# Performance work log

Measured on AMD Instinct MI355X. Metric: run time of the kernel, lower is better.

The kernel has to match this reference:

```python
import jax, jax.numpy as jnp
import numpy as np

PAD, BOS = 0, 1
EPS = 1e-08


def _lstm_cell(xt, h, c, wih, whh, bih, bhh):
    z = xt @ wih.T + h @ whh.T + bih + bhh
    i, f, g, o = jnp.split(z, 4, axis=-1)  # torch gate order i,f,g,o
    c = jax.nn.sigmoid(f) * c + jax.nn.sigmoid(i) * jnp.tanh(g)
    h = jax.nn.sigmoid(o) * jnp.tanh(c)
    return h, c


def _run_lstm(emb, wih, whh, bih, bhh):
    B, H = emb.shape[0], whh.shape[1]
    def step(carry, xt):
        h, c = _lstm_cell(xt, carry[0], carry[1], wih, whh, bih, bhh)
        return (h, c), h
    init = (jnp.zeros((B, H), emb.dtype), jnp.zeros((B, H), emb.dtype))
    (hT, cT), outs = jax.lax.scan(step, init, jnp.swapaxes(emb, 0, 1))
    return jnp.swapaxes(outs, 0, 1), hT, cT


def setup_inputs() -> dict:
    key = jax.random.key(0)
    V, H, B, S, T = 32000, 256, 8, 200, 51
    ks = jax.random.split(key, 24)
    def n(i, shape, s=0.02):
        return jax.random.normal(ks[i], shape, jnp.float32) * s
    x = jax.random.randint(ks[0], (B, S), 1, V)
    x = x.at[:, -1].set(V - 1)  # pins extended vocab size to 2V
    labels = jax.random.randint(ks[1], (B, T), 1, V)
    return {
        "x": x, "labels": labels, "ext_vocab_size": 2 * V,
        "emb_enc": n(2, (V, H)).at[PAD].set(0.0),
        "wih_f": n(3, (4 * H, H)), "whh_f": n(4, (4 * H, H)),
        "bih_f": jnp.zeros((4 * H,), jnp.float32), "bhh_f": jnp.zeros((4 * H,), jnp.float32),
        "wih_b": n(5, (4 * H, H)), "whh_b": n(6, (4 * H, H)),
        "bih_b": jnp.zeros((4 * H,), jnp.float32), "bhh_b": jnp.zeros((4 * H,), jnp.float32),
        "w_sel1": n(7, (H, 2 * H)), "b_sel1": jnp.zeros((H,), jnp.float32),
        "w_sel2": n(8, (1, H)), "b_sel2": jnp.zeros((1,), jnp.float32),
        "w_rh": n(9, (H, 2 * H)), "b_rh": jnp.zeros((H,), jnp.float32),
        "w_rc": n(10, (H, 2 * H)), "b_rc": jnp.zeros((H,), jnp.float32),
        "emb_dec": n(11, (V, H)).at[PAD].set(0.0),
        "wih_d": n(12, (4 * H, 3 * H)), "whh_d": n(13, (4 * H, H)),
        "bih_d": jnp.zeros((4 * H,), jnp.float32), "bhh_d": jnp.zeros((4 * H,), jnp.float32),
        "w_attn": n(14, (H, 4 * H)), "b_attn": jnp.zeros((H,), jnp.float32),
        "w_attn_v": n(15, (1, H)),
        "w_ptr": n(16, (1, 3 * H)), "b_ptr": jnp.zeros((1,), jnp.float32),
        "w_gen": n(17, (V, H)), "b_gen": jnp.zeros((V,), jnp.float32),
        "w_cov": n(18, (H, 1)), "b_cov": jnp.zeros((H,), jnp.float32),
    }


def reference(x, labels, ext_vocab_size, emb_enc, wih_f, whh_f, bih_f, bhh_f,
              wih_b, whh_b, bih_b, bhh_b, w_sel1, b_sel1, w_sel2, b_sel2,
              w_rh, b_rh, w_rc, b_rc, emb_dec, wih_d, whh_d, bih_d, bhh_d,
              w_attn, b_attn, w_attn_v, w_ptr, b_ptr, w_gen, b_gen, w_cov, b_cov):
    B, S = x.shape
    V, H = w_gen.shape
    # ---- Encoder: BiLSTM (no padding -> packing is identity; eval -> no dropout)
    emb = emb_enc[x]  # [B,S,H]
    out_f, h_f, c_f = _run_lstm(emb, wih_f, whh_f, bih_f, bhh_f)
    out_b_r, h_b, c_b = _run_lstm(emb[:, ::-1], wih_b, whh_b, bih_b, bhh_b)
    enc_out = jnp.concatenate([out_f, out_b_r[:, ::-1]], axis=-1)  # [B,S,2H]
    copy_probs = jax.nn.sigmoid(
        (jnp.tanh(enc_out @ w_sel1.T + b_sel1) @ w_sel2.T + b_sel2)[..., 0])  # [B,S]
    # ---- bidirectional state reduction
    h0 = jax.nn.relu(jnp.concatenate([h_f, h_b], -1) @ w_rh.T + b_rh)
    c0 = jax.nn.relu(jnp.concatenate([c_f, c_b], -1) @ w_rc.T + b_rc)
    # ---- Decoder loop (teacher forcing): inputs = [BOS, labels[:,1:T-1]]
    dec_in = jnp.concatenate(
        [jnp.full((B, 1), BOS, labels.dtype), labels[:, 1:-1]], axis=1)  # [B,T-1]
    mask_cp = (copy_probs > EPS).astype(jnp.float32)
    rows = jnp.arange(B)[:, None]

    def step(carry, tok):
        h, c, cov = carry
        cov_feat = cov[..., None] * w_cov[:, 0] + b_cov  # [B,S,H]
        feats = jnp.concatenate(
            [enc_out, jnp.broadcast_to(h[:, None, :], (B, S, H)), cov_feat], axis=-1)
        e = jnp.tanh(feats @ w_attn.T + b_attn)           # [B,S,H]
        attn = jax.nn.softmax(e @ w_attn_v[0], axis=1)    # [B,S]
        attn = attn * mask_cp
        attn = attn / (attn.sum(1, keepdims=True) + 1e-10)
        cov = cov + attn
        ctx = jnp.einsum('bs,bsd->bd', attn, enc_out)     # [B,2H]
        h, c = _lstm_cell(jnp.concatenate([emb_dec[tok], ctx], -1), h, c,
                          wih_d, whh_d, bih_d, bhh_d)
        p_gen = jax.nn.sigmoid(jnp.concatenate([ctx, h], -1) @ w_ptr.T + b_ptr)  # [B,1]
        vocab_dist = jax.nn.softmax(h @ w_gen.T + b_gen, axis=-1)  # [B,V]
        dist = jnp.zeros((B, ext_vocab_size), jnp.float32)
        dist = dist.at[:, :V].set(p_gen * vocab_dist)
        dist = dist.at[rows, x].add((1.0 - p_gen) * attn)  # pointer/copy scatter-add
        return (h, c, cov), dist

    cov0 = jnp.zeros((B, S), jnp.float32)
    _, outs = jax.lax.scan(step, (h0, c0, cov0), dec_in.T)
    outputs = jnp.swapaxes(outs, 0, 1)  # [B,T-1,EV]
    # ---- loss (faithful: CE treats the mixture distribution as logits)
    targets = labels[:, 1:]
    logp = jax.nn.log_softmax(outputs, axis=-1)
    nll = -jnp.take_along_axis(logp, targets[..., None], axis=-1)[..., 0]
    valid = (targets != PAD).astype(jnp.float32)
    loss_ce = (nll * valid).sum() / valid.sum()
    m = (x != PAD).astype(jnp.float32)
    lp = jnp.clip(jnp.log(copy_probs), -100.0, None)
    l1p = jnp.clip(jnp.log1p(-copy_probs), -100.0, None)
    bce = -(m * lp + (1.0 - m) * l1p)
    loss = loss_ce + 1.0 * (bce * m).sum() / m.sum()
    return outputs, loss
```

## Files before the change

### kernel.cpp

```cpp
#include <hip/hip_runtime.h>
#include <hip/hip_bf16.h>
#include <stdint.h>


#define DEVI __device__ __forceinline__
#define AT_RLX __ATOMIC_RELAXED
#define SC_AGT __HIP_MEMORY_SCOPE_AGENT

static constexpr size_t OFF_ACC   = 0;
static constexpr size_t OFF_FLAGE = 4;
static constexpr size_t OFF_FLAGD = 36;
static constexpr size_t ZERO_FLOATS = 200;
static constexpr size_t OFF_CTX   = 256;
static constexpr size_t OFF_EMB   = 4352;
static constexpr size_t OFF_HSEL  = OFF_EMB;
static constexpr size_t OFF_HP    = OFF_EMB;
static constexpr size_t OFF_PREF  = OFF_EMB  + 409600;
static constexpr size_t OFF_PREB  = OFF_PREF + 1638400;
static constexpr size_t OFF_BIAS  = OFF_PREB + 1638400;
static constexpr size_t OFF_HB    = OFF_BIAS + 3072;
static constexpr size_t OFF_HFIN  = OFF_HB   + 8192;
static constexpr size_t OFF_CFIN  = OFF_HFIN + 4096;
static constexpr size_t OFF_ENCOUT= OFF_CFIN + 4096;
static constexpr size_t OFF_MASK  = OFF_ENCOUT + 819200;
static constexpr size_t OFF_C0    = OFF_MASK + 1600;
static constexpr size_t OFF_EP    = OFF_C0   + 2048;
static constexpr size_t OFF_WCP   = OFF_EP   + 409600;
static constexpr size_t OFF_BCP   = OFF_WCP  + 256;
static constexpr size_t OFF_DEMB  = OFF_BCP  + 256;
static constexpr size_t OFF_DPRE  = OFF_DEMB + 102400;
static constexpr size_t OFF_HBUF  = OFF_DPRE + 409600;
static constexpr size_t OFF_CS    = OFF_HBUF + 4096;
static constexpr size_t OFF_HS    = OFF_CS   + 204800;
static constexpr size_t OFF_AS    = OFF_HS   + 102400;
static constexpr size_t OFF_PG    = OFF_AS   + 80000;
static constexpr size_t OFF_PE    = OFF_PG   + 512;

DEVI float sigf(float x)      { return 1.0f / (1.0f + __expf(-x)); }
DEVI float tanh_fast(float x) { return 1.0f - 2.0f / (1.0f + __expf(2.0f * x)); }
DEVI float ald(const float* p)  { return __hip_atomic_load((float*)p, AT_RLX, SC_AGT); }
DEVI void  ast(float* p, float v){ __hip_atomic_store(p, v, AT_RLX, SC_AGT); }

DEVI void fbar(int* flags, int g, int n, int val) {
  __syncthreads();
  if ((int)threadIdx.x == 0)
    __hip_atomic_store(flags + g, val, AT_RLX, SC_AGT);
  if ((int)threadIdx.x < n && (int)threadIdx.x != g) {
    while (__hip_atomic_load(flags + threadIdx.x, AT_RLX, SC_AGT) < val)
      __builtin_amdgcn_s_sleep(1);
  }
  __syncthreads();
}

__global__ __launch_bounds__(256) void k_biassum(
    const float* bih_f, const float* bhh_f, const float* bih_b, const float* bhh_b,
    const float* bih_d, const float* bhh_d, float* ws) {
  int i = blockIdx.x * 256 + threadIdx.x;
  int which = i >> 10, jj = i & 1023;
  float v = (which == 0) ? bih_f[jj] + bhh_f[jj]
          : (which == 1) ? bih_b[jj] + bhh_b[jj]
                         : bih_d[jj] + bhh_d[jj];
  ws[OFF_BIAS + i] = v;
}

__global__ __launch_bounds__(256) void k_embed(
    const int* xin, const int* labels, const float* emb_enc, const float* emb_dec, float* ws) {
  int r = blockIdx.x, h = threadIdx.x;
  if (r < 1600) {
    int t = r >> 3, b = r & 7;
    ws[OFF_EMB + (size_t)r * 256 + h] = emb_enc[(size_t)xin[b * 200 + t] * 256 + h];
  } else {
    int r2 = r - 1600;
    int t = r2 >> 3, b = r2 & 7;
    int tok = (t == 0) ? 1 : labels[b * 51 + t];
    ws[OFF_DEMB + (size_t)r2 * 256 + h] = emb_dec[(size_t)tok * 256 + h];
  }
}

template<int BM, int BN, int TM, int TN, int CMAP, int ACT, int AMAP>
__global__ __launch_bounds__(256) void k_gemm(
    const float* __restrict__ A, const float* __restrict__ B,
    const float* __restrict__ bias, float* __restrict__ C,
    int M, int K, int ldb, int ldc) {
  __shared__ float As[16][BM];
  __shared__ float Bs[16][BN];
  const int tid = threadIdx.x;
  const int tx = tid & 15, ty = tid >> 4;
  const int m0 = blockIdx.x * BM, n0 = blockIdx.y * BN;
  float acc[TM][TN];
#pragma unroll
  for (int i = 0; i < TM; ++i)
#pragma unroll
    for (int q = 0; q < TN; ++q) acc[i][q] = 0.f;

  for (int kk = 0; kk < K; kk += 16) {
#pragma unroll
    for (int e = tid; e < BM * 4; e += 256) {
      int m = e >> 2, k4 = (e & 3) * 4;
      int gm0 = m0 + m;
      float4 v = {0.f, 0.f, 0.f, 0.f};
      if (gm0 < M) {
        int gm = AMAP ? (((199 - (gm0 >> 3)) << 3) + (gm0 & 7)) : gm0;
        v = *(const float4*)(A + (size_t)gm * K + kk + k4);
      }
      As[k4 + 0][m] = v.x; As[k4 + 1][m] = v.y; As[k4 + 2][m] = v.z; As[k4 + 3][m] = v.w;
    }
#pragma unroll
    for (int e = tid; e < BN * 4; e += 256) {
      int n = e >> 2, k4 = (e & 3) * 4;
      float4 v = *(const float4*)(B + (size_t)(n0 + n) * ldb + kk + k4);
      Bs[k4 + 0][n] = v.x; Bs[k4 + 1][n] = v.y; Bs[k4 + 2][n] = v.z; Bs[k4 + 3][n] = v.w;
    }
    __syncthreads();
#pragma unroll
    for (int k = 0; k < 16; ++k) {
      float a[TM], bv[TN];
#pragma unroll
      for (int i = 0; i < TM; ++i) a[i] = As[k][ty * TM + i];
#pragma unroll
      for (int q = 0; q < TN; ++q) bv[q] = Bs[k][tx * TN + q];
#pragma unroll
      for (int i = 0; i < TM; ++i)
#pragma unroll
        for (int q = 0; q < TN; ++q) acc[i][q] += a[i] * bv[q];
    }
    __syncthreads();
  }
#pragma unroll
  for (int i = 0; i < TM; ++i) {
    int gm = m0 + ty * TM + i;
    if (gm >= M) continue;
    size_t base;
    if (CMAP == 1) { int t = gm >> 3, b = gm & 7; base = (size_t)(b * 50 + t) * 64000; }
    else            base = (size_t)gm * ldc;
#pragma unroll
    for (int q = 0; q < TN; ++q) {
      int n = n0 + tx * TN + q;
      float v = acc[i][q] + bias[n];
      if (ACT == 1) v = tanh_fast(v);
      C[base + n] = v;
    }
  }
}

__global__ __launch_bounds__(512, 1) void k_encoder(
    const float* __restrict__ whh_f, const float* __restrict__ whh_b, float* __restrict__ ws) {
  __shared__ float hs[8 * 288];
  __shared__ float zs[512];
  const int dir = blockIdx.x >> 4;
  const int p   = blockIdx.x & 15;
  const int u0  = p * 16;
  const float* whh = dir ? whh_b : whh_f;
  const float* pre = ws + (dir ? OFF_PREB : OFF_PREF);
  unsigned long long* hp = (unsigned long long*)(ws + OFF_HP);
  const int tid = threadIdx.x;
  const int r = tid >> 3, kc = tid & 7;
  const int gt = r >> 4, ui = r & 15;
  const int j = gt * 256 + u0 + ui;
  float4 W[8];
  {
    const float* wr = whh + (size_t)j * 256 + kc * 32;
#pragma unroll
    for (int q = 0; q < 8; ++q) W[q] = *(const float4*)(wr + q * 4);
  }
  const int ui2 = tid & 15, b2 = tid >> 4;
  float c_reg = 0.f;
  float* enc = ws + OFF_ENCOUT;

  for (int t = 0; t < 200; ++t) {
    float pre_v = pre[((size_t)t * 8 + kc) * 1024 + j];
    float acc[8];
#pragma unroll
    for (int b = 0; b < 8; ++b) acc[b] = 0.f;
    if (t > 0) {
      {
        unsigned long long* src = hp + (size_t)((((t + 1) & 1) * 2 + dir) * 2048) + tid * 4;
        const unsigned long long e = (unsigned long long)(unsigned)t;
        unsigned long long a0, a1, a2, a3;
        for (;;) {
          a0 = __hip_atomic_load(src + 0, AT_RLX, SC_AGT);
          a1 = __hip_atomic_load(src + 1, AT_RLX, SC_AGT);
          a2 = __hip_atomic_load(src + 2, AT_RLX, SC_AGT);
          a3 = __hip_atomic_load(src + 3, AT_RLX, SC_AGT);
          if (((a0 >> 32) == e) && ((a1 >> 32) == e) &&
              ((a2 >> 32) == e) && ((a3 >> 32) == e)) break;
          __builtin_amdgcn_s_sleep(1);
        }
        int kk0 = (tid * 4) & 255, bb = tid >> 6;
        float* dst = &hs[bb * 288 + (kk0 >> 5) * 36 + (kk0 & 31)];
        dst[0] = __uint_as_float((unsigned)a0);
        dst[1] = __uint_as_float((unsigned)a1);
        dst[2] = __uint_as_float((unsigned)a2);
        dst[3] = __uint_as_float((unsigned)a3);
      }
      __syncthreads();
      const float* hrow = &hs[kc * 36];
#pragma unroll
      for (int b = 0; b < 8; ++b) {
        const float* hbp = hrow + b * 288;
#pragma unroll
        for (int q = 0; q < 8; ++q) {
          float4 h4 = *(const float4*)(hbp + q * 4);
          acc[b] = fmaf(W[q].x, h4.x, acc[b]);
          acc[b] = fmaf(W[q].y, h4.y, acc[b]);
          acc[b] = fmaf(W[q].z, h4.z, acc[b]);
          acc[b] = fmaf(W[q].w, h4.w, acc[b]);
        }
      }
    }
    {
      bool h4b = (kc & 4) != 0;
#pragma unroll
      for (int i = 0; i < 4; ++i) {
        float send = h4b ? acc[i] : acc[i + 4];
        float keep = h4b ? acc[i + 4] : acc[i];
        acc[i] = keep + __shfl_xor(send, 4);
      }
      bool h2b = (kc & 2) != 0;
#pragma unroll
      for (int i = 0; i < 2; ++i) {
        float send = h2b ? acc[i] : acc[i + 2];
        float keep = h2b ? acc[i + 2] : acc[i];
        acc[i] = keep + __shfl_xor(send, 2);
      }
      bool h1b = (kc & 1) != 0;
      {
        float send = h1b ? acc[0] : acc[1];
        float keep = h1b ? acc[1] : acc[0];
        acc[0] = keep + __shfl_xor(send, 1);
      }
    }
    zs[tid] = acc[0] + pre_v;
    __syncthreads();
    if (tid < 128) {
      int i0 = ui2 * 8 + b2;
      float zi = zs[i0], zf = zs[128 + i0], zg = zs[256 + i0], zo = zs[384 + i0];
      float cn = sigf(zf) * c_reg + sigf(zi) * tanh_fast(zg);
      float hn = sigf(zo) * tanh_fast(cn);
      c_reg = cn;
      int uu = u0 + ui2;
      if (t < 199) {
        unsigned long long pk =
            ((unsigned long long)(unsigned)(t + 1) << 32) |
            (unsigned long long)__float_as_uint(hn);
        __hip_atomic_store(hp + (size_t)(((t & 1) * 2 + dir) * 2048) + b2 * 256 + uu,
                           pk, AT_RLX, SC_AGT);
      }
      int s = dir ? (199 - t) : t;
      enc[((size_t)b2 * 200 + s) * 512 + dir * 256 + uu] = hn;
      if (t == 199) {
        ws[OFF_HFIN + (size_t)(dir * 8 + b2) * 256 + uu] = hn;
        ws[OFF_CFIN + (size_t)(dir * 8 + b2) * 256 + uu] = cn;
      }
    }
  }
}

__global__ __launch_bounds__(64) void k_selbce(
    const float* w_sel2, const float* b_sel2, const int* xin, float* ws) {
  int r = blockIdx.x, lane = threadIdx.x;
  float pacc = 0.f;
#pragma unroll
  for (int i = 0; i < 4; ++i) {
    int k = lane + 64 * i;
    pacc += ws[OFF_HSEL + (size_t)r * 256 + k] * w_sel2[k];
  }
#pragma unroll
  for (int m = 1; m < 64; m <<= 1) pacc += __shfl_xor(pacc, m);
  if (lane == 0) {
    float cp = sigf(pacc + b_sel2[0]);
    ws[OFF_MASK + r] = (cp > 1e-8f) ? 1.f : 0.f;
    int b = r / 200, s = r % 200;
    float m = (xin[b * 200 + s] != 0) ? 1.f : 0.f;
    if (m > 0.f) {
      float lp = fmaxf(logf(cp), -100.f);
      atomicAdd(ws + OFF_ACC + 2, -lp);
    }
    atomicAdd(ws + OFF_ACC + 3, m);
  }
}

__global__ __launch_bounds__(256) void k_wcp(
    const float* w_attn, const float* w_cov, const float* b_cov, float* ws) {
  int jj = threadIdx.x;
  float a = 0.f, c = 0.f;
  for (int h = 0; h < 256; ++h) {
    float w = w_attn[(size_t)jj * 1024 + 768 + h];
    a += w * w_cov[h];
    c += w * b_cov[h];
  }
  ws[OFF_WCP + jj] = a;
  ws[OFF_BCP + jj] = c;
}

__global__ __launch_bounds__(256) void k_h0c0(
    const float* w_rh, const float* b_rh, const float* w_rc, const float* b_rc, float* ws) {
  int b = blockIdx.x, jj = threadIdx.x;
  const float* hf  = ws + OFF_HFIN + (size_t)b * 256;
  const float* hbk = ws + OFF_HFIN + 2048 + (size_t)b * 256;
  const float* cf  = ws + OFF_CFIN + (size_t)b * 256;
  const float* cbk = ws + OFF_CFIN + 2048 + (size_t)b * 256;
  float ah = b_rh[jj], ac = b_rc[jj];
  for (int k = 0; k < 256; ++k) {
    ah += hf[k] * w_rh[(size_t)jj * 512 + k];
    ac += cf[k] * w_rc[(size_t)jj * 512 + k];
  }
  for (int k = 0; k < 256; ++k) {
    ah += hbk[k] * w_rh[(size_t)jj * 512 + 256 + k];
    ac += cbk[k] * w_rc[(size_t)jj * 512 + 256 + k];
  }
  ws[OFF_C0 + (size_t)b * 256 + jj] = fmaxf(ac, 0.f);
  ws[OFF_HBUF + (size_t)b * 256 + jj] = fmaxf(ah, 0.f);
}

__global__ __launch_bounds__(512, 1) void k_decoder(
    const float* __restrict__ wih_d, const float* __restrict__ whh_d,
    const float* __restrict__ w_attn, const float* __restrict__ w_attn_v,
    float* __restrict__ ws) {
  __shared__ float hc_s[8 * 768];
  __shared__ float h_pad[264];
  __shared__ float hw_q[64];
  __shared__ float e_s[256];
  __shared__ float at_s[256], cv_s[256], msk_s[256];
  __shared__ float zs_l[256];
  __shared__ float wcq_s[64], bcq_s[64], wvq_s[64];
  __shared__ float mS_s[2];
  const int g = blockIdx.x, tid = threadIdx.x;
  const int b1 = g >> 2, sq = g & 3, s0 = sq * 50;
  int* flags = (int*)(ws + OFF_FLAGD);
  const int jl = tid >> 3, kq = tid & 7;
  const int kseg = tid & 15, row_l = tid >> 4;
  const int u_l = row_l & 7, gate = row_l >> 3;
  const int j = gate * 256 + g * 8 + u_l;
  float4 W48[12];
#pragma unroll
  for (int q = 0; q < 12; ++q) {
    int k0 = 4 * kseg + 64 * q;
    W48[q] = (k0 < 512) ? *(const float4*)(wih_d + (size_t)j * 768 + 256 + k0)
                        : *(const float4*)(whh_d + (size_t)j * 256 + (k0 - 512));
  }
  float4 W32[8];
  {
    const float* wsrc = w_attn + (size_t)(sq * 64 + jl) * 1024 + 512 + kq * 32;
#pragma unroll
    for (int q = 0; q < 8; ++q) W32[q] = *(const float4*)(wsrc + q * 4);
  }
  const int u_c = tid & 7, b_c = tid >> 3;
  float c_reg = (tid < 64) ? ws[OFF_C0 + (size_t)b_c * 256 + g * 8 + u_c] : 0.f;
  for (int s = tid; s < 256; s += 512) {
    msk_s[s] = (s < 200) ? ws[OFF_MASK + b1 * 200 + s] : 0.f;
    cv_s[s] = 0.f;
  }
  if (tid < 64) {
    wcq_s[tid] = ws[OFF_WCP + sq * 64 + tid];
    bcq_s[tid] = ws[OFF_BCP + sq * 64 + tid];
    wvq_s[tid] = w_attn_v[sq * 64 + tid];
  }
  __syncthreads();

  for (int t = 0; t < 50; ++t) {
    const int rb = t & 1, wb = 1 - rb;
    if (tid < 128) ast(ws + OFF_CTX + g * 128 + tid, 0.f);
    if (tid < 256) {
      float v = ald(ws + OFF_HBUF + (size_t)rb * 2048 + b1 * 256 + tid);
      h_pad[(tid >> 5) * 33 + (tid & 31)] = v;
    }
    __syncthreads();
    {
      float a = 0.f;
      const float* hq = &h_pad[kq * 33];
#pragma unroll
      for (int q = 0; q < 8; ++q) {
        float4 h4 = { hq[q * 4 + 0], hq[q * 4 + 1], hq[q * 4 + 2], hq[q * 4 + 3] };
        a = fmaf(W32[q].x, h4.x, a);
        a = fmaf(W32[q].y, h4.y, a);
        a = fmaf(W32[q].z, h4.z, a);
        a = fmaf(W32[q].w, h4.w, a);
      }
      a += __shfl_xor(a, 1);
      a += __shfl_xor(a, 2);
      a += __shfl_xor(a, 4);
      if (kq == 0) hw_q[jl] = a;
    }
    __syncthreads();
    if (tid < 200) {
      const int s = tid;
      float cv = cv_s[s];
      const float* ep = ws + OFF_EP + ((size_t)(b1 * 200 + s)) * 256 + sq * 64;
      float pe = 0.f;
#pragma unroll
      for (int i4 = 0; i4 < 16; ++i4) {
        float4 e4 = *(const float4*)(ep + i4 * 4);
        float4 h4 = *(const float4*)(&hw_q[i4 * 4]);
        float4 w4 = *(const float4*)(&wcq_s[i4 * 4]);
        float4 b4 = *(const float4*)(&bcq_s[i4 * 4]);
        float4 v4 = *(const float4*)(&wvq_s[i4 * 4]);
        pe = fmaf(tanh_fast(e4.x + h4.x + cv * w4.x + b4.x), v4.x, pe);
        pe = fmaf(tanh_fast(e4.y + h4.y + cv * w4.y + b4.y), v4.y, pe);
        pe = fmaf(tanh_fast(e4.z + h4.z + cv * w4.z + b4.z), v4.z, pe);
        pe = fmaf(tanh_fast(e4.w + h4.w + cv * w4.w + b4.w), v4.w, pe);
      }
      ast(ws + OFF_PE + (size_t)(sq * 8 + b1) * 200 + s, pe);
    }
    fbar(flags, g, 32, 3 * t + 1);

    if (tid < 200) {
      float e0 = ald(ws + OFF_PE + (size_t)(0 * 8 + b1) * 200 + tid);
      float e1 = ald(ws + OFF_PE + (size_t)(1 * 8 + b1) * 200 + tid);
      float e2 = ald(ws + OFF_PE + (size_t)(2 * 8 + b1) * 200 + tid);
      float e3 = ald(ws + OFF_PE + (size_t)(3 * 8 + b1) * 200 + tid);
      e_s[tid] = (e0 + e1) + (e2 + e3);
    }
    __syncthreads();
    if (tid < 64) {
      float m = -1e30f;
#pragma unroll
      for (int i = 0; i < 4; ++i) {
        int s = tid + 64 * i;
        if (s < 200) m = fmaxf(m, e_s[s]);
      }
#pragma unroll
      for (int md = 1; md < 64; md <<= 1) m = fmaxf(m, __shfl_xor(m, md));
      float es = 0.f, ems = 0.f;
#pragma unroll
      for (int i = 0; i < 4; ++i) {
        int s = tid + 64 * i;
        if (s < 200) {
          float e = __expf(e_s[s] - m);
          es += e; ems += e * msk_s[s];
        }
      }
#pragma unroll
      for (int md = 1; md < 64; md <<= 1) { es += __shfl_xor(es, md); ems += __shfl_xor(ems, md); }
      if (tid == 0) { mS_s[0] = m; mS_s[1] = 1.0f / (ems + 1e-10f * es); }
    }
    __syncthreads();
    if (tid < 200) {
      float a = __expf(e_s[tid] - mS_s[0]) * msk_s[tid] * mS_s[1];
      at_s[tid] = a;
      cv_s[tid] += a;
      if (tid >= s0 && tid < s0 + 50)
        ws[OFF_AS + ((size_t)t * 8 + b1) * 200 + tid] = a;
    }
    __syncthreads();
    {
      float ca = 0.f;
      const float* ebase = ws + OFF_ENCOUT + ((size_t)(b1 * 200 + s0)) * 512 + tid;
#pragma unroll 10
      for (int s2 = 0; s2 < 50; ++s2)
        ca = fmaf(at_s[s0 + s2], ebase[(size_t)s2 * 512], ca);
      atomicAdd(ws + OFF_CTX + b1 * 512 + tid, ca);
    }
    fbar(flags, g, 32, 3 * t + 2);

    for (int e = tid; e < 6144; e += 512) {
      int bb = e / 768, kk2 = e % 768;
      hc_s[e] = (kk2 < 512) ? ald(ws + OFF_CTX + bb * 512 + kk2)
                            : ald(ws + OFF_HBUF + (size_t)rb * 2048 + bb * 256 + (kk2 - 512));
    }
    __syncthreads();
    if (g < 8) ws[OFF_CS + ((size_t)t * 8 + g) * 512 + tid] = hc_s[g * 768 + tid];
    float acc[8];
#pragma unroll
    for (int b = 0; b < 8; ++b) acc[b] = 0.f;
#pragma unroll
    for (int q = 0; q < 12; ++q) {
      int k0 = 4 * kseg + 64 * q;
#pragma unroll
      for (int b = 0; b < 8; ++b) {
        float4 h4 = *(const float4*)(&hc_s[b * 768 + k0]);
        acc[b] = fmaf(W48[q].x, h4.x, acc[b]);
        acc[b] = fmaf(W48[q].y, h4.y, acc[b]);
        acc[b] = fmaf(W48[q].z, h4.z, acc[b]);
        acc[b] = fmaf(W48[q].w, h4.w, acc[b]);
      }
    }
    {
      bool h8 = (kseg & 8) != 0;
#pragma unroll
      for (int i = 0; i < 4; ++i) {
        float send = h8 ? acc[i] : acc[i + 4];
        float keep = h8 ? acc[i + 4] : acc[i];
        acc[i] = keep + __shfl_xor(send, 8);
      }
      bool h4b = (kseg & 4) != 0;
#pragma unroll
      for (int i = 0; i < 2; ++i) {
        float send = h4b ? acc[i] : acc[i + 2];
        float keep = h4b ? acc[i + 2] : acc[i];
        acc[i] = keep + __shfl_xor(send, 4);
      }
      bool h2b = (kseg & 2) != 0;
      {
        float send = h2b ? acc[0] : acc[1];
        float keep = h2b ? acc[1] : acc[0];
        acc[0] = keep + __shfl_xor(send, 2);
      }
      acc[0] += __shfl_xor(acc[0], 1);
    }
    {
      int bz = kseg >> 1;
      float z = acc[0] + ws[OFF_DPRE + ((size_t)t * 8 + bz) * 1024 + j];
      if ((kseg & 1) == 0) zs_l[row_l * 8 + bz] = z;
    }
    __syncthreads();
    if (tid < 64) {
      float zi = zs_l[(0  + u_c) * 8 + b_c];
      float zf = zs_l[(8  + u_c) * 8 + b_c];
      float zg = zs_l[(16 + u_c) * 8 + b_c];
      float zo = zs_l[(24 + u_c) * 8 + b_c];
      float cn = sigf(zf) * c_reg + sigf(zi) * tanh_fast(zg);
      float hn = sigf(zo) * tanh_fast(cn);
      c_reg = cn;
      ast(ws + OFF_HBUF + (size_t)wb * 2048 + b_c * 256 + g * 8 + u_c, hn);
      ws[OFF_HS + ((size_t)t * 8 + b_c) * 256 + g * 8 + u_c] = hn;
    }
    fbar(flags, g, 32, 3 * t + 3);
  }
}

__global__ __launch_bounds__(64) void k_pgen(const float* w_ptr, const float* b_ptr, float* ws) {
  int r = blockIdx.x, lane = threadIdx.x;
  float p = 0.f;
#pragma unroll
  for (int i = 0; i < 12; ++i) {
    int k = lane + 64 * i;
    float v = (k < 512) ? ws[OFF_CS + (size_t)r * 512 + k]
                        : ws[OFF_HS + (size_t)r * 256 + (k - 512)];
    p += v * w_ptr[k];
  }
#pragma unroll
  for (int m = 1; m < 64; m <<= 1) p += __shfl_xor(p, m);
  if (lane == 0) ws[OFF_PG + r] = sigf(p + b_ptr[0]);
}

__global__ __launch_bounds__(256) void k_v2(const int* xin, const int* labels, float* ws, float* out) {
  __shared__ float redm[256], reds[256];
  __shared__ int xv[200];
  __shared__ float s1sh, corrsh;
  int r = blockIdx.x, tid = threadIdx.x;
  int tt = r >> 3, b = r & 7;
  float* row = out + (size_t)(b * 50 + tt) * 64000;
  for (int i = tid; i < 200; i += 256) xv[i] = xin[b * 200 + i];
  float m = -1e30f, s = 0.f;
  for (int i = tid; i < 32000; i += 256) {
    float z = row[i];
    float nm = fmaxf(m, z);
    s = s * __expf(m - nm) + __expf(z - nm);
    m = nm;
  }
  redm[tid] = m; reds[tid] = s;
  __syncthreads();
  for (int st = 128; st >= 1; st >>= 1) {
    if (tid < st) {
      float m2 = redm[tid + st], s2 = reds[tid + st];
      float M = fmaxf(redm[tid], m2);
      reds[tid] = reds[tid] * __expf(redm[tid] - M) + s2 * __expf(m2 - M);
      redm[tid] = M;
    }
    __syncthreads();
  }
  float mx = redm[0], sum = reds[0];
  float pg = ws[OFF_PG + r];
  __syncthreads();
  float s1 = 0.f;
  float inv = 1.0f / sum;
  for (int i = tid; i < 32000; i += 256) {
    float z = row[i];
    float d = pg * (__expf(z - mx) * inv);
    row[i] = d;
    s1 += __expf(d);
  }
  for (int i = 32000 + tid; i < 64000; i += 256) row[i] = 0.0f;
  reds[tid] = s1;
  __syncthreads();
  for (int st = 128; st >= 1; st >>= 1) { if (tid < st) reds[tid] += reds[tid + st]; __syncthreads(); }
  if (tid == 0) { s1sh = reds[0]; corrsh = 0.f; }
  __syncthreads();
  if (tid < 200) {
    int v = xv[tid];
    bool own = true;
    for (int s2 = 0; s2 < tid; ++s2) if (xv[s2] == v) { own = false; break; }
    if (own) {
      float delta = 0.f;
      for (int s2 = tid; s2 < 200; ++s2)
        if (xv[s2] == v) delta += ws[OFF_AS + (size_t)r * 200 + s2];
      delta *= (1.0f - pg);
      float base = row[v];
      row[v] = base + delta;
      atomicAdd(&corrsh, __expf(base + delta) - __expf(base));
    }
  }
  __syncthreads();
  if (tid == 0) {
    float lse = logf(s1sh + corrsh + 32000.0f);
    int tgt = labels[b * 51 + tt + 1];
    float dt = row[tgt];
    float valid = (tgt != 0) ? 1.f : 0.f;
    atomicAdd(ws + OFF_ACC + 0, valid * (lse - dt));
    atomicAdd(ws + OFF_ACC + 1, valid);
  }
}

__global__ void k_loss(float* ws, float* out, int out_size) {
  out[out_size - 1] = ws[OFF_ACC + 0] / ws[OFF_ACC + 1] + ws[OFF_ACC + 2] / ws[OFF_ACC + 3];
}

extern "C" void kernel_launch(void* const* d_in, const int* in_sizes, int n_in,
                              void* d_out, int out_size, void* d_ws, size_t ws_size,
                              hipStream_t stream) {
  (void)in_sizes; (void)n_in; (void)ws_size;
  const int*   x       = (const int*)  d_in[0];
  const int*   labels  = (const int*)  d_in[1];
  const float* emb_enc = (const float*)d_in[3];
  const float* wih_f   = (const float*)d_in[4];
  const float* whh_f   = (const float*)d_in[5];
  const float* bih_f   = (const float*)d_in[6];
  const float* bhh_f   = (const float*)d_in[7];
  const float* wih_b   = (const float*)d_in[8];
  const float* whh_b   = (const float*)d_in[9];
  const float* bih_b   = (const float*)d_in[10];
  const float* bhh_b   = (const float*)d_in[11];
  const float* w_sel1  = (const float*)d_in[12];
  const float* b_sel1  = (const float*)d_in[13];
  const float* w_sel2  = (const float*)d_in[14];
  const float* b_sel2  = (const float*)d_in[15];
  const float* w_rh    = (const float*)d_in[16];
  const float* b_rh    = (const float*)d_in[17];
  const float* w_rc    = (const float*)d_in[18];
  const float* b_rc    = (const float*)d_in[19];
  const float* emb_dec = (const float*)d_in[20];
  const float* wih_d   = (const float*)d_in[21];
  const float* whh_d   = (const float*)d_in[22];
  const float* bih_d   = (const float*)d_in[23];
  const float* bhh_d   = (const float*)d_in[24];
  const float* w_attn  = (const float*)d_in[25];
  const float* b_attn  = (const float*)d_in[26];
  const float* w_attn_v= (const float*)d_in[27];
  const float* w_ptr   = (const float*)d_in[28];
  const float* b_ptr   = (const float*)d_in[29];
  const float* w_gen   = (const float*)d_in[30];
  const float* b_gen   = (const float*)d_in[31];
  const float* w_cov   = (const float*)d_in[32];
  const float* b_cov   = (const float*)d_in[33];
  float* ws  = (float*)d_ws;
  float* out = (float*)d_out;

  hipMemsetAsync(d_ws, 0, ZERO_FLOATS * 4, stream);
  k_biassum<<<12, 256, 0, stream>>>(bih_f, bhh_f, bih_b, bhh_b, bih_d, bhh_d, ws);
  k_embed<<<2000, 256, 0, stream>>>(x, labels, emb_enc, emb_dec, ws);
  k_gemm<64,64,4,4,0,0,0><<<dim3(25,16), 256, 0, stream>>>(ws+OFF_EMB,  wih_f, ws+OFF_BIAS,      ws+OFF_PREF, 1600, 256, 256, 1024);
  k_gemm<64,64,4,4,0,0,1><<<dim3(25,16), 256, 0, stream>>>(ws+OFF_EMB,  wih_b, ws+OFF_BIAS+1024, ws+OFF_PREB, 1600, 256, 256, 1024);
  k_gemm<64,64,4,4,0,0,0><<<dim3(7,16),  256, 0, stream>>>(ws+OFF_DEMB, wih_d, ws+OFF_BIAS+2048, ws+OFF_DPRE, 400,  256, 768, 1024);
  hipMemsetAsync((void*)(ws + OFF_HP), 0, (size_t)2 * 2 * 2048 * sizeof(unsigned long long), stream);
  k_encoder<<<32, 512, 0, stream>>>(whh_f, whh_b, ws);
  k_gemm<64,64,4,4,0,1,0><<<dim3(25,4),  256, 0, stream>>>(ws+OFF_ENCOUT, w_sel1, b_sel1, ws+OFF_HSEL, 1600, 512, 512, 256);
  k_selbce<<<1600, 64, 0, stream>>>(w_sel2, b_sel2, x, ws);
  k_gemm<64,64,4,4,0,0,0><<<dim3(25,4),  256, 0, stream>>>(ws+OFF_ENCOUT, w_attn, b_attn, ws+OFF_EP, 1600, 512, 1024, 256);
  k_wcp<<<1, 256, 0, stream>>>(w_attn, w_cov, b_cov, ws);
  k_h0c0<<<8, 256, 0, stream>>>(w_rh, b_rh, w_rc, b_rc, ws);
  k_decoder<<<32, 512, 0, stream>>>(wih_d, whh_d, w_attn, w_attn_v, ws);
  k_pgen<<<400, 64, 0, stream>>>(w_ptr, b_ptr, ws);
  k_gemm<128,128,8,8,1,0,0><<<dim3(4,250), 256, 0, stream>>>(ws+OFF_HS, w_gen, b_gen, out, 400, 256, 256, 64000);
  k_v2<<<400, 256, 0, stream>>>(x, labels, ws, out);
  k_loss<<<1, 1, 0, stream>>>(ws, out, out_size);
}
```

Measured before the change: 2.314 ms.

## Remap encoder recurrence threads to two gate rows and sixteen k-chunks

Restructures the encoder LSTM recurrent matvec so each thread holds two weight rows over a 16-wide k-slice instead of one row over 32, and reuses each shared-memory h vector load for both rows. The shared h buffer gets an interleaved layout, and the butterfly reduction grows an extra shuffle stage over 16 lanes. The aim is to halve LDS reads per FMA on the serial 200-step critical path, at the cost of more accumulator registers and an extra shuffle level.

```diff
diff --git a/kernel.cpp b/kernel.cpp
--- a/kernel.cpp
+++ b/kernel.cpp
@@ -145,7 +145,7 @@
 
 __global__ __launch_bounds__(512, 1) void k_encoder(
     const float* __restrict__ whh_f, const float* __restrict__ whh_b, float* __restrict__ ws) {
-  __shared__ float hs[8 * 288];
+  __shared__ float hs2[2048];
   __shared__ float zs[512];
   const int dir = blockIdx.x >> 4;
   const int p   = blockIdx.x & 15;
@@ -154,83 +154,104 @@
   const float* pre = ws + (dir ? OFF_PREB : OFF_PREF);
   unsigned long long* hp = (unsigned long long*)(ws + OFF_HP);
   const int tid = threadIdx.x;
-  const int r = tid >> 3, kc = tid & 7;
-  const int gt = r >> 4, ui = r & 15;
-  const int j = gt * 256 + u0 + ui;
-  float4 W[8];
+  const int kc4 = tid & 15;
+  const int jp  = tid >> 4;
+  const int jj0 = jp * 2, jj1 = jj0 + 1;
+  const int jg0 = (jj0 >> 4) * 256 + u0 + (jj0 & 15);
+  const int jg1 = (jj1 >> 4) * 256 + u0 + (jj1 & 15);
+  float4 W0[4], W1[4];
   {
-    const float* wr = whh + (size_t)j * 256 + kc * 32;
-#pragma unroll
-    for (int q = 0; q < 8; ++q) W[q] = *(const float4*)(wr + q * 4);
-  }
+    const float* w0 = whh + (size_t)jg0 * 256 + kc4 * 16;
+    const float* w1 = whh + (size_t)jg1 * 256 + kc4 * 16;
+#pragma unroll
+    for (int q = 0; q < 4; ++q) { W0[q] = *(const float4*)(w0 + q * 4);
+                                  W1[q] = *(const float4*)(w1 + q * 4); }
+  }
+  const int jlf = kc4 >> 3, bf = kc4 & 7;
+  const int jjf = jp * 2 + jlf;
+  const int jf  = (jjf >> 4) * 256 + u0 + (jjf & 15);
+  const int zsl = (jjf >> 4) * 128 + (jjf & 15) * 8 + bf;
+  const int wb_ = tid >> 6;
+  const int kk0 = (tid * 4) & 255;
+  const int wdst = wb_ * 256 + ((kk0 >> 2) & 3) * 64 + (kk0 >> 4) * 4;
   const int ui2 = tid & 15, b2 = tid >> 4;
   float c_reg = 0.f;
   float* enc = ws + OFF_ENCOUT;
 
   for (int t = 0; t < 200; ++t) {
-    float pre_v = pre[((size_t)t * 8 + kc) * 1024 + j];
-    float acc[8];
-#pragma unroll
-    for (int b = 0; b < 8; ++b) acc[b] = 0.f;
+    float pre_v = pre[((size_t)t * 8 + bf) * 1024 + jf];
+    float acc[16];
+#pragma unroll
+    for (int i = 0; i < 16; ++i) acc[i] = 0.f;
     if (t > 0) {
-      {
-        unsigned long long* src = hp + (size_t)((((t + 1) & 1) * 2 + dir) * 2048) + tid * 4;
-        const unsigned long long e = (unsigned long long)(unsigned)t;
-        unsigned long long a0, a1, a2, a3;
-        for (;;) {
-          a0 = __hip_atomic_load(src + 0, AT_RLX, SC_AGT);
-          a1 = __hip_atomic_load(src + 1, AT_RLX, SC_AGT);
-          a2 = __hip_atomic_load(src + 2, AT_RLX, SC_AGT);
-          a3 = __hip_atomic_load(src + 3, AT_RLX, SC_AGT);
-          if (((a0 >> 32) == e) && ((a1 >> 32) == e) &&
-              ((a2 >> 32) == e) && ((a3 >> 32) == e)) break;
-          __builtin_amdgcn_s_sleep(1);
+      unsigned long long* src = hp + (size_t)((((t + 1) & 1) * 2 + dir) * 2048) + tid * 4;
+      const unsigned long long e = (unsigned long long)(unsigned)t;
+      unsigned long long a0, a1, a2, a3;
+      for (;;) {
+        a0 = __hip_atomic_load(src + 0, AT_RLX, SC_AGT);
+        a1 = __hip_atomic_load(src + 1, AT_RLX, SC_AGT);
+        a2 = __hip_atomic_load(src + 2, AT_RLX, SC_AGT);
+        a3 = __hip_atomic_load(src + 3, AT_RLX, SC_AGT);
+        if (((a0 >> 32) == e) && ((a1 >> 32) == e) &&
+            ((a2 >> 32) == e) && ((a3 >> 32) == e)) break;
+        __builtin_amdgcn_s_sleep(1);
+      }
+      float4 hv;
+      hv.x = __uint_as_float((unsigned)a0);
+      hv.y = __uint_as_float((unsigned)a1);
+      hv.z = __uint_as_float((unsigned)a2);
+      hv.w = __uint_as_float((unsigned)a3);
+      *(float4*)(&hs2[wdst]) = hv;
+    }
+    __syncthreads();
+    if (t > 0) {
+#pragma unroll
+      for (int b = 0; b < 8; ++b) {
+        const float* hb = &hs2[b * 256 + kc4 * 4];
+#pragma unroll
+        for (int q = 0; q < 4; ++q) {
+          float4 h4 = *(const float4*)(hb + q * 64);
+          acc[b]     = fmaf(W0[q].x, h4.x, acc[b]);
+          acc[b]     = fmaf(W0[q].y, h4.y, acc[b]);
+          acc[b]     = fmaf(W0[q].z, h4.z, acc[b]);
+          acc[b]     = fmaf(W0[q].w, h4.w, acc[b]);
+          acc[8 + b] = fmaf(W1[q].x, h4.x, acc[8 + b]);
+          acc[8 + b] = fmaf(W1[q].y, h4.y, acc[8 + b]);
+          acc[8 + b] = fmaf(W1[q].z, h4.z, acc[8 + b]);
+          acc[8 + b] = fmaf(W1[q].w, h4.w, acc[8 + b]);
         }
-        int kk0 = (tid * 4) & 255, bb = tid >> 6;
-        float* dst = &hs[bb * 288 + (kk0 >> 5) * 36 + (kk0 & 31)];
-        dst[0] = __uint_as_float((unsigned)a0);
-        dst[1] = __uint_as_float((unsigned)a1);
-        dst[2] = __uint_as_float((unsigned)a2);
-        dst[3] = __uint_as_float((unsigned)a3);
-      }
-      __syncthreads();
-      const float* hrow = &hs[kc * 36];
-#pragma unroll
-      for (int b = 0; b < 8; ++b) {
-        const float* hbp = hrow + b * 288;
-#pragma unroll
-        for (int q = 0; q < 8; ++q) {
-          float4 h4 = *(const float4*)(hbp + q * 4);
-          acc[b] = fmaf(W[q].x, h4.x, acc[b]);
-          acc[b] = fmaf(W[q].y, h4.y, acc[b]);
-          acc[b] = fmaf(W[q].z, h4.z, acc[b]);
-          acc[b] = fmaf(W[q].w, h4.w, acc[b]);
-        }
       }
     }
     {
-      bool h4b = (kc & 4) != 0;
+      bool h8 = (kc4 & 8) != 0;
+#pragma unroll
+      for (int i = 0; i < 8; ++i) {
+        float send = h8 ? acc[i] : acc[i + 8];
+        float keep = h8 ? acc[i + 8] : acc[i];
+        acc[i] = keep + __shfl_xor(send, 8);
+      }
+      bool h4b = (kc4 & 4) != 0;
 #pragma unroll
       for (int i = 0; i < 4; ++i) {
         float send = h4b ? acc[i] : acc[i + 4];
         float keep = h4b ? acc[i + 4] : acc[i];
         acc[i] = keep + __shfl_xor(send, 4);
       }
-      bool h2b = (kc & 2) != 0;
+      bool h2b = (kc4 & 2) != 0;
 #pragma unroll
       for (int i = 0; i < 2; ++i) {
         float send = h2b ? acc[i] : acc[i + 2];
         float keep = h2b ? acc[i + 2] : acc[i];
         acc[i] = keep + __shfl_xor(send, 2);
       }
-      bool h1b = (kc & 1) != 0;
+      bool h1b = (kc4 & 1) != 0;
       {
         float send = h1b ? acc[0] : acc[1];
         float keep = h1b ? acc[1] : acc[0];
         acc[0] = keep + __shfl_xor(send, 1);
       }
     }
-    zs[tid] = acc[0] + pre_v;
+    zs[zsl] = acc[0] + pre_v;
     __syncthreads();
     if (tid < 128) {
       int i0 = ui2 * 8 + b2;
```

Result: faster. 2.073 ms (-10.4%).
